# Kernel tuning notes

Measured on AMD Instinct MI355X. Metric: run time of the kernel, lower is better.

The kernel has to match this reference:

```python
import jax, jax.numpy as jnp
import numpy as np

DIM = 192
NUM_HEADS = 6
WH, WW = 7, 7
N = WH * WW  # 49 tokens per window
C2 = 2 * DIM  # concatenated channel dim = 384
SCALE = (DIM // NUM_HEADS) ** -0.5  # module uses dim//num_heads, not C2//num_heads
NW = 64  # number of windows per image
B_ = 2048  # num_windows * batch


def _relative_position_index():
    ch = np.arange(WH)
    cw = np.arange(WW)
    coords = np.stack(np.meshgrid(ch, cw, indexing='ij')).reshape(2, -1)  # [2, N]
    rel = coords[:, :, None] - coords[:, None, :]  # [2, N, N]
    rel = rel.transpose(1, 2, 0).astype(np.int64)  # [N, N, 2]
    rel[..., 0] += WH - 1
    rel[..., 1] += WW - 1
    rel[..., 0] *= 2 * WW - 1
    return jnp.asarray(rel.sum(-1))  # [N, N]

REL_IDX = _relative_position_index()


def setup_inputs() -> dict:
    key = jax.random.key(0)
    ks = jax.random.split(key, 8)
    x = jax.random.normal(ks[0], (B_, N, DIM), dtype=jnp.float32)
    y = jax.random.normal(ks[1], (B_, N, DIM), dtype=jnp.float32)
    mask = jax.random.normal(ks[2], (NW, N, N), dtype=jnp.float32)
    w_qkv = jax.random.normal(ks[3], (6 * DIM, C2), dtype=jnp.float32) * 0.02
    b_qkv = jnp.zeros((6 * DIM,), dtype=jnp.float32)
    w_proj = jax.random.normal(ks[4], (DIM, C2), dtype=jnp.float32) * 0.02
    b_proj = jnp.zeros((DIM,), dtype=jnp.float32)
    bias_table = jax.random.normal(ks[5], ((2 * WH - 1) * (2 * WW - 1), NUM_HEADS), dtype=jnp.float32) * 0.02
    return {"x": x, "y": y, "mask": mask, "w_qkv": w_qkv, "b_qkv": b_qkv,
            "w_proj": w_proj, "b_proj": b_proj, "bias_table": bias_table}


def reference(x, y, mask, w_qkv, b_qkv, w_proj, b_proj, bias_table):
    Bc = x.shape[0]
    Dh = C2 // NUM_HEADS  # 64
    xy = jnp.concatenate([x, y], axis=2)  # [B_, N, 2*dim]
    qkv = xy @ w_qkv.T + b_qkv  # [B_, N, 6*dim]
    qkv = qkv.reshape(Bc, N, 3, NUM_HEADS, Dh).transpose(2, 0, 3, 1, 4)  # [3, B_, H, N, Dh]
    q, k, v = qkv[0] * SCALE, qkv[1], qkv[2]
    attn = jnp.einsum('bhnd,bhmd->bhnm', q, k)  # [B_, H, N, N]
    rpb = bias_table[REL_IDX]  # [N, N, H]
    attn = attn + rpb.transpose(2, 0, 1)[None]
    nW = mask.shape[0]
    attn = attn.reshape(Bc // nW, nW, NUM_HEADS, N, N) + mask[None, :, None]
    attn = attn.reshape(Bc, NUM_HEADS, N, N)
    attn = jax.nn.softmax(attn, axis=-1)
    out = jnp.einsum('bhnm,bhmd->bhnd', attn, v)  # [B_, H, N, Dh]
    out = out.transpose(0, 2, 1, 3).reshape(Bc, N, C2)
    return out @ w_proj.T + b_proj  # [B_, N, dim]
```

## Files before the change

### kernel.cpp

```cpp
#include <hip/hip_runtime.h>
#include <hip/hip_bf16.h>


typedef __attribute__((ext_vector_type(8))) short short8;
typedef __attribute__((ext_vector_type(4))) float f32x4;

#define SCALE 0.17677669529663687f

#define WQF_OFF    0ul
#define WQF_BYTES  (864ul*1024)
#define WPF_OFF    (WQF_OFF + WQF_BYTES)
#define WPF_BYTES  (144ul*1024)
#define COMB_OFF   (WPF_OFF + WPF_BYTES)
#define COMB_BYTES (64ul*6*4096*4)
#define XYF_OFF    (COMB_OFF + COMB_BYTES)
#define XYF_BYTES  (2048ul*48*1024)
#define OF_OFF     (XYF_OFF + XYF_BYTES)
#define OF_BYTES   XYF_BYTES
#define WS_NEED    (OF_OFF + OF_BYTES)

__device__ __forceinline__ unsigned short f2bf(float f){
  unsigned u = __builtin_bit_cast(unsigned, f);
  u = u + 0x7fffu + ((u >> 16) & 1u);
  return (unsigned short)(u >> 16);
}
__device__ __forceinline__ unsigned long long pack4(float4 v){
  return (unsigned long long)f2bf(v.x) | ((unsigned long long)f2bf(v.y) << 16)
       | ((unsigned long long)f2bf(v.z) << 32) | ((unsigned long long)f2bf(v.w) << 48);
}

__global__ void k0_wfrag(const float* __restrict__ wq_f, const float* __restrict__ wp_f,
                         unsigned short* __restrict__ wqf, unsigned short* __restrict__ wpf){
  int t = blockIdx.x*256 + threadIdx.x;
  int fragidx = t >> 6, l = t & 63;
  const float* src; unsigned short* dst;
  if (fragidx < 864){
    int h = fragidx/144, rem = fragidx - h*144;
    int ct = rem/12, kt = rem - ct*12;
    int row = (ct>>2)*384 + h*64 + (ct&3)*16 + (l&15);
    src = wq_f + (long)row*384 + kt*32 + (l>>4)*8;
    dst = wqf + (long)fragidx*512 + l*8;
  } else {
    int fid = fragidx - 864;
    int ct = fid/12, kt = fid - ct*12;
    int row = ct*16 + (l&15);
    src = wp_f + (long)row*384 + kt*32 + (l>>4)*8;
    dst = wpf + (long)fid*512 + l*8;
  }
  short8 v;
  #pragma unroll
  for (int e = 0; e < 8; ++e) v[e] = (short)f2bf(src[e]);
  *(short8*)dst = v;
}

__global__ void prep_comb(const float* __restrict__ mask, const float* __restrict__ btab,
                          float* __restrict__ comb){
  int idx = blockIdx.x * 256 + threadIdx.x;
  int j = idx & 63, i = (idx >> 6) & 63, rest = idx >> 12;
  int h = rest % 6, w = rest / 6;
  float v;
  if (i < 49 && j < 49){
    int di = i / 7 - j / 7 + 6;
    int dj = i % 7 - j % 7 + 6;
    v = btab[(di * 13 + dj) * 6 + h] + mask[(w * 49 + i) * 49 + j];
  } else {
    v = (j >= 49) ? -1e30f : 0.0f;
  }
  comb[idx] = v;
}

__global__ void k1_xyfrag(const float* __restrict__ x, const float* __restrict__ y,
                          unsigned short* __restrict__ xyf){
  const int kt  = blockIdx.x;
  const int win = blockIdx.y;
  const int mt  = threadIdx.x >> 6;
  const int l   = threadIdx.x & 63;
  const int row = mt*16 + (l & 15);
  const int c0  = kt*32 + (l >> 4)*8;
  short8 v = {};
  if (row < 49){
    const float* src = (kt < 6) ? (x + ((long)win*49 + row)*192 + c0)
                                : (y + ((long)win*49 + row)*192 + (c0 - 192));
    float4 f0 = *(const float4*)src, f1 = *(const float4*)(src+4);
    unsigned long long lo = pack4(f0), hi = pack4(f1);
    #pragma unroll
    for (int e = 0; e < 4; ++e){ v[e] = (short)(lo >> (16*e)); v[4+e] = (short)(hi >> (16*e)); }
  }
  *(short8*)(xyf + (((long)win*12 + kt)*4 + mt)*512 + l*8) = v;
}

__device__ __forceinline__ int swz(int r, int b){ return b ^ ((r & 7) << 4); }
__device__ __forceinline__ int a_q (int r, int c){ return 0     + swz(r, r*128 + c*2); }
__device__ __forceinline__ int a_k (int r, int c){ return 8192  + swz(r, r*128 + c*2); }
__device__ __forceinline__ int a_vt(int r, int c){ return 16384 + swz(r, r*128 + c*2); }
__device__ __forceinline__ int a_p (int r, int c){ return 24576 + swz(r, r*128 + c*2); }

__global__ __launch_bounds__(256, 3)
void k2_qkv_attn(const unsigned short* __restrict__ xyf, const unsigned short* __restrict__ wqf,
                 const float* __restrict__ bqkv, const float* __restrict__ comb,
                 unsigned short* __restrict__ Of){
  __shared__ __align__(16) unsigned char smem[32768];
  const int h = blockIdx.x, win = blockIdx.y;
  const int tid = threadIdx.x, w = tid>>6, l = tid&63, l15 = l&15, lg = l>>4;

  const float* cb = comb + ((long)((win & 63)*6 + h))*4096;
  float cbv[16];
  #pragma unroll
  for (int j = 0; j < 4; ++j)
    #pragma unroll
    for (int nt = 0; nt < 4; ++nt)
      cbv[j*4+nt] = cb[(w*16 + lg*4 + j)*64 + nt*16 + l15];
  float bias[3];
  #pragma unroll
  for (int nt = 0; nt < 3; ++nt){
    int n = w*48 + nt*16 + l15;
    bias[nt] = bqkv[(n>>6)*384 + h*64 + (n&63)];
  }

  f32x4 acc[4][3] = {};
  const unsigned short* Ab = xyf + (long)win*24576;
  const unsigned short* Bb = wqf + ((long)h*12 + w*3)*12*512;
  #pragma unroll 3
  for (int kt = 0; kt < 12; ++kt){
    short8 a[4];
    #pragma unroll
    for (int mt = 0; mt < 4; ++mt)
      a[mt] = *(const short8*)(Ab + (kt*4 + mt)*512 + l*8);
    #pragma unroll
    for (int nt = 0; nt < 3; ++nt){
      short8 bb = *(const short8*)(Bb + (nt*12 + kt)*512 + l*8);
      #pragma unroll
      for (int mt = 0; mt < 4; ++mt)
        acc[mt][nt] = __builtin_amdgcn_mfma_f32_16x16x32_bf16(a[mt], bb, acc[mt][nt], 0, 0, 0);
    }
  }
  #pragma unroll
  for (int nt = 0; nt < 3; ++nt){
    int ct = w*3 + nt, s = ct>>2, d = (ct&3)*16 + l15;
    #pragma unroll
    for (int mt = 0; mt < 4; ++mt){
      #pragma unroll
      for (int j = 0; j < 4; ++j){
        int row = mt*16 + lg*4 + j;
        float v = acc[mt][nt][j] + bias[nt];
        if (s == 0) v *= SCALE;
        int addr = (s==0) ? a_q(row,d) : (s==1) ? a_k(row,d) : a_vt(d,row);
        *(unsigned short*)(smem + addr) = f2bf(v);
      }
    }
  }
  __syncthreads();

  short8 aq[2];
  #pragma unroll
  for (int ks = 0; ks < 2; ++ks)
    aq[ks] = *(const short8*)(smem + a_q(w*16 + l15, ks*32 + lg*8));
  f32x4 sacc[4] = {};
  #pragma unroll
  for (int ks = 0; ks < 2; ++ks){
    #pragma unroll
    for (int nt = 0; nt < 4; ++nt){
      short8 bk = *(const short8*)(smem + a_k(nt*16 + l15, ks*32 + lg*8));
      sacc[nt] = __builtin_amdgcn_mfma_f32_16x16x32_bf16(aq[ks], bk, sacc[nt], 0, 0, 0);
    }
  }
  float rs[4];
  #pragma unroll
  for (int j = 0; j < 4; ++j){
    int r = w*16 + lg*4 + j;
    #pragma unroll
    for (int nt = 0; nt < 4; ++nt)
      sacc[nt][j] += cbv[j*4+nt];
    float m = fmaxf(fmaxf(sacc[0][j], sacc[1][j]), fmaxf(sacc[2][j], sacc[3][j]));
    #pragma unroll
    for (int dlt = 1; dlt < 16; dlt <<= 1) m = fmaxf(m, __shfl_xor(m, dlt));
    float ssum = 0.f;
    #pragma unroll
    for (int nt = 0; nt < 4; ++nt){
      float e = __expf(sacc[nt][j] - m);
      sacc[nt][j] = e;
      ssum += e;
    }
    #pragma unroll
    for (int dlt = 1; dlt < 16; dlt <<= 1) ssum += __shfl_xor(ssum, dlt);
    rs[j] = ssum;
    #pragma unroll
    for (int nt = 0; nt < 4; ++nt)
      *(unsigned short*)(smem + a_p(r, nt*16 + l15)) = f2bf(sacc[nt][j]);
  }
  short8 ap[2];
  #pragma unroll
  for (int ks = 0; ks < 2; ++ks)
    ap[ks] = *(const short8*)(smem + a_p(w*16 + l15, ks*32 + lg*8));
  f32x4 oacc[4] = {};
  #pragma unroll
  for (int ks = 0; ks < 2; ++ks){
    #pragma unroll
    for (int nt = 0; nt < 4; ++nt){
      short8 bv = *(const short8*)(smem + a_vt(nt*16 + l15, ks*32 + lg*8));
      oacc[nt] = __builtin_amdgcn_mfma_f32_16x16x32_bf16(ap[ks], bv, oacc[nt], 0, 0, 0);
    }
  }
  float inv[4];
  #pragma unroll
  for (int j = 0; j < 4; ++j) inv[j] = 1.0f / rs[j];
  #pragma unroll
  for (int nt = 0; nt < 4; ++nt){
    #pragma unroll
    for (int j = 0; j < 4; ++j){
      int row = w*16 + lg*4 + j;
      *(unsigned short*)(smem + a_p(row, nt*16 + l15)) = f2bf(oacc[nt][j] * inv[j]);
    }
  }
  unsigned short* Ob = Of + (((long)win*12 + h*2)*4 + w)*512 + l*8;
  #pragma unroll
  for (int ks = 0; ks < 2; ++ks){
    short8 o8 = *(const short8*)(smem + a_p(w*16 + l15, ks*32 + lg*8));
    *(short8*)(Ob + ks*4*512) = o8;
  }
}

__global__ __launch_bounds__(256, 4)
void k3_proj(const unsigned short* __restrict__ Of, const unsigned short* __restrict__ wpf,
             const float* __restrict__ bproj, float* __restrict__ out){
  const int win = blockIdx.x;
  const int tid = threadIdx.x, w = tid>>6, l = tid&63, l15 = l&15, lg = l>>4;
  float bp[3]; int np[3];
  #pragma unroll
  for (int nt = 0; nt < 3; ++nt){
    np[nt] = w*48 + nt*16 + l15;
    bp[nt] = bproj[np[nt]];
  }
  f32x4 acc[4][3] = {};
  const unsigned short* Ab = Of + (long)win*24576;
  const unsigned short* Bb = wpf + (long)(w*3)*12*512;
  #pragma unroll 3
  for (int kt = 0; kt < 12; ++kt){
    short8 a[4];
    #pragma unroll
    for (int mt = 0; mt < 4; ++mt)
      a[mt] = *(const short8*)(Ab + (kt*4 + mt)*512 + l*8);
    #pragma unroll
    for (int nt = 0; nt < 3; ++nt){
      short8 bb = *(const short8*)(Bb + (nt*12 + kt)*512 + l*8);
      #pragma unroll
      for (int mt = 0; mt < 4; ++mt)
        acc[mt][nt] = __builtin_amdgcn_mfma_f32_16x16x32_bf16(a[mt], bb, acc[mt][nt], 0, 0, 0);
    }
  }
  #pragma unroll
  for (int mt = 0; mt < 4; ++mt){
    #pragma unroll
    for (int j = 0; j < 4; ++j){
      int row = mt*16 + lg*4 + j;
      if (row < 49){
        float* o = out + ((long)win*49 + row)*192;
        #pragma unroll
        for (int nt = 0; nt < 3; ++nt)
          o[np[nt]] = acc[mt][nt][j] + bp[nt];
      }
    }
  }
}

#define FB_WQ_ELEMS (1152*384)
#define FB_WP_ELEMS (192*384)
#define FB_WP_OFF   (FB_WQ_ELEMS*2)
#define FB_COMB_OFF (FB_WP_OFF + FB_WP_ELEMS*2)

__global__ void prep_weights_fb(const float* __restrict__ wq_f, const float* __restrict__ wp_f,
                                unsigned short* __restrict__ wq, unsigned short* __restrict__ wp){
  int gid = blockIdx.x * 256 + threadIdx.x;
  if (gid < FB_WQ_ELEMS) wq[gid] = f2bf(wq_f[gid]);
  else { int g = gid - FB_WQ_ELEMS; if (g < FB_WP_ELEMS) wp[g] = f2bf(wp_f[g]); }
}
__device__ __forceinline__ int fb_xy(int r, int c){ return 0      + swz(r, r*768 + c*2); }
__device__ __forceinline__ int fb_q (int r, int c){ return 49152  + swz(r, r*128 + c*2); }
__device__ __forceinline__ int fb_k (int r, int c){ return 57344  + swz(r, r*128 + c*2); }
__device__ __forceinline__ int fb_vt(int r, int c){ return 65536  + swz(r, r*128 + c*2); }
__device__ __forceinline__ int fb_p (int r, int c){ return 73728  + swz(r, r*128 + c*2); }

__global__ __launch_bounds__(256, 2)
void fused_attn_fb(const float* __restrict__ x, const float* __restrict__ y,
                   const float* __restrict__ bqkv, const float* __restrict__ bproj,
                   const unsigned short* __restrict__ wq, const unsigned short* __restrict__ wp,
                   const float* __restrict__ comb, float* __restrict__ out){
  __shared__ __align__(16) unsigned char smem[81920];
  const int b = blockIdx.x, tid = threadIdx.x;
  const int w = tid>>6, l = tid&63, l15 = l&15, lg = l>>4;
  {
    const float4* x4 = (const float4*)x + b * 2352;
    const float4* y4 = (const float4*)y + b * 2352;
    for (int idx = tid; idx < 2352; idx += 256){
      int r = idx / 48, c4 = (idx % 48) * 4;
      float4 vx = x4[idx], vy = y4[idx];
      *(unsigned long long*)(smem + fb_xy(r, c4))       = pack4(vx);
      *(unsigned long long*)(smem + fb_xy(r, 192 + c4)) = pack4(vy);
    }
    for (int idx = tid; idx < 1440; idx += 256){
      int r = 49 + idx / 96, c4 = (idx % 96) * 4;
      *(unsigned long long*)(smem + fb_xy(r, c4)) = 0ull;
    }
  }
  __syncthreads();
  const float* cbB = comb + (long)(b & 63) * (6 * 4096);
  f32x4 pacc[4][3] = {};
  int np[3]; float bp[3];
  #pragma unroll
  for (int nt = 0; nt < 3; ++nt){ np[nt] = w*48 + nt*16 + l15; bp[nt] = bproj[np[nt]]; }
  #pragma unroll 1
  for (int h = 0; h < 6; ++h){
    f32x4 acc[4][3] = {};
    int wrow[3]; float bias[3];
    #pragma unroll
    for (int nt = 0; nt < 3; ++nt){
      int n = np[nt];
      wrow[nt] = (n >> 6) * 384 + h * 64 + (n & 63);
      bias[nt] = bqkv[wrow[nt]];
    }
    #pragma unroll 4
    for (int kt = 0; kt < 12; ++kt){
      int k0 = kt * 32;
      short8 a[4];
      #pragma unroll
      for (int mt = 0; mt < 4; ++mt)
        a[mt] = *(const short8*)(smem + fb_xy(mt*16 + l15, k0 + lg*8));
      #pragma unroll
      for (int nt = 0; nt < 3; ++nt){
        short8 bb = *(const short8*)(wq + (long)wrow[nt]*384 + k0 + lg*8);
        #pragma unroll
        for (int mt = 0; mt < 4; ++mt)
          acc[mt][nt] = __builtin_amdgcn_mfma_f32_16x16x32_bf16(a[mt], bb, acc[mt][nt], 0, 0, 0);
      }
    }
    #pragma unroll
    for (int nt = 0; nt < 3; ++nt){
      int n = np[nt], s = n >> 6, d = n & 63;
      #pragma unroll
      for (int mt = 0; mt < 4; ++mt){
        #pragma unroll
        for (int j = 0; j < 4; ++j){
          int row = mt*16 + lg*4 + j;
          float v = acc[mt][nt][j] + bias[nt];
          if (s == 0) v *= SCALE;
          int addr = (s==0) ? fb_q(row,d) : (s==1) ? fb_k(row,d) : fb_vt(d,row);
          *(unsigned short*)(smem + addr) = f2bf(v);
        }
      }
    }
    __syncthreads();
    short8 aq[2];
    #pragma unroll
    for (int ks = 0; ks < 2; ++ks)
      aq[ks] = *(const short8*)(smem + fb_q(w*16 + l15, ks*32 + lg*8));
    f32x4 sacc[4] = {};
    #pragma unroll
    for (int ks = 0; ks < 2; ++ks)
      #pragma unroll
      for (int nt = 0; nt < 4; ++nt){
        short8 bk = *(const short8*)(smem + fb_k(nt*16 + l15, ks*32 + lg*8));
        sacc[nt] = __builtin_amdgcn_mfma_f32_16x16x32_bf16(aq[ks], bk, sacc[nt], 0, 0, 0);
      }
    const float* cb = cbB + h * 4096;
    float rs[4];
    #pragma unroll
    for (int j = 0; j < 4; ++j){
      int r = w*16 + lg*4 + j;
      #pragma unroll
      for (int nt = 0; nt < 4; ++nt) sacc[nt][j] += cb[r*64 + nt*16 + l15];
      float m = fmaxf(fmaxf(sacc[0][j], sacc[1][j]), fmaxf(sacc[2][j], sacc[3][j]));
      #pragma unroll
      for (int dlt = 1; dlt < 16; dlt <<= 1) m = fmaxf(m, __shfl_xor(m, dlt));
      float ssum = 0.f;
      #pragma unroll
      for (int nt = 0; nt < 4; ++nt){
        float e = __expf(sacc[nt][j] - m);
        sacc[nt][j] = e; ssum += e;
      }
      #pragma unroll
      for (int dlt = 1; dlt < 16; dlt <<= 1) ssum += __shfl_xor(ssum, dlt);
      rs[j] = ssum;
      #pragma unroll
      for (int nt = 0; nt < 4; ++nt)
        *(unsigned short*)(smem + fb_p(r, nt*16 + l15)) = f2bf(sacc[nt][j]);
    }
    short8 ap[2];
    #pragma unroll
    for (int ks = 0; ks < 2; ++ks)
      ap[ks] = *(const short8*)(smem + fb_p(w*16 + l15, ks*32 + lg*8));
    f32x4 oacc[4] = {};
    #pragma unroll
    for (int ks = 0; ks < 2; ++ks)
      #pragma unroll
      for (int nt = 0; nt < 4; ++nt){
        short8 bv = *(const short8*)(smem + fb_vt(nt*16 + l15, ks*32 + lg*8));
        oacc[nt] = __builtin_amdgcn_mfma_f32_16x16x32_bf16(ap[ks], bv, oacc[nt], 0, 0, 0);
      }
    float inv[4];
    #pragma unroll
    for (int j = 0; j < 4; ++j) inv[j] = 1.0f / rs[j];
    #pragma unroll
    for (int nt = 0; nt < 4; ++nt)
      #pragma unroll
      for (int j = 0; j < 4; ++j){
        int row = w*16 + lg*4 + j;
        *(unsigned short*)(smem + fb_p(row, nt*16 + l15)) = f2bf(oacc[nt][j] * inv[j]);
      }
    __syncthreads();
    #pragma unroll
    for (int ks = 0; ks < 2; ++ks){
      short8 ao8[4];
      #pragma unroll
      for (int mt = 0; mt < 4; ++mt)
        ao8[mt] = *(const short8*)(smem + fb_p(mt*16 + l15, ks*32 + lg*8));
      #pragma unroll
      for (int nt = 0; nt < 3; ++nt){
        short8 bb = *(const short8*)(wp + (long)np[nt]*384 + h*64 + ks*32 + lg*8);
        #pragma unroll
        for (int mt = 0; mt < 4; ++mt)
          pacc[mt][nt] = __builtin_amdgcn_mfma_f32_16x16x32_bf16(ao8[mt], bb, pacc[mt][nt], 0, 0, 0);
      }
    }
  }
  #pragma unroll
  for (int mt = 0; mt < 4; ++mt)
    #pragma unroll
    for (int j = 0; j < 4; ++j){
      int row = mt*16 + lg*4 + j;
      if (row < 49){
        float* o = out + ((long)b*49 + row)*192;
        #pragma unroll
        for (int nt = 0; nt < 3; ++nt)
          o[np[nt]] = pacc[mt][nt][j] + bp[nt];
      }
    }
}

extern "C" void kernel_launch(void* const* d_in, const int* in_sizes, int n_in,
                              void* d_out, int out_size, void* d_ws, size_t ws_size,
                              hipStream_t stream){
  (void)in_sizes; (void)n_in; (void)out_size;
  const float* x     = (const float*)d_in[0];
  const float* y     = (const float*)d_in[1];
  const float* mask  = (const float*)d_in[2];
  const float* wq_f  = (const float*)d_in[3];
  const float* bqkv  = (const float*)d_in[4];
  const float* wp_f  = (const float*)d_in[5];
  const float* bproj = (const float*)d_in[6];
  const float* btab  = (const float*)d_in[7];
  float* out = (float*)d_out;

  if (ws_size >= WS_NEED){
    unsigned short* wqf = (unsigned short*)((char*)d_ws + WQF_OFF);
    unsigned short* wpf = (unsigned short*)((char*)d_ws + WPF_OFF);
    float*          cmb = (float*)((char*)d_ws + COMB_OFF);
    unsigned short* xyf = (unsigned short*)((char*)d_ws + XYF_OFF);
    unsigned short* Ofr = (unsigned short*)((char*)d_ws + OF_OFF);
    hipLaunchKernelGGL(k0_wfrag,    dim3(252),     dim3(256), 0, stream, wq_f, wp_f, wqf, wpf);
    hipLaunchKernelGGL(prep_comb,   dim3(6144),    dim3(256), 0, stream, mask, btab, cmb);
    hipLaunchKernelGGL(k1_xyfrag,   dim3(12,2048), dim3(256), 0, stream, x, y, xyf);
    hipLaunchKernelGGL(k2_qkv_attn, dim3(6,2048),  dim3(256), 0, stream, xyf, wqf, bqkv, cmb, Ofr);
    hipLaunchKernelGGL(k3_proj,     dim3(2048),    dim3(256), 0, stream, Ofr, wpf, bproj, out);
  } else {
    unsigned short* wq  = (unsigned short*)d_ws;
    unsigned short* wp  = (unsigned short*)((char*)d_ws + FB_WP_OFF);
    float*          cmb = (float*)((char*)d_ws + FB_COMB_OFF);
    hipLaunchKernelGGL(prep_weights_fb, dim3(2016), dim3(256), 0, stream, wq_f, wp_f, wq, wp);
    hipLaunchKernelGGL(prep_comb,       dim3(6144), dim3(256), 0, stream, mask, btab, cmb);
    hipLaunchKernelGGL(fused_attn_fb,   dim3(2048), dim3(256), 0, stream,
                       x, y, bqkv, bproj, wq, wp, cmb, out);
  }
}
```

Before: 275.4 us.

## Transpose score MFMA, reuse Q smem for P, raise occupancy, remap blocks across XCDs

The attention kernel now computes S^T via swapped MFMA operands, so each lane holds a full column of scores. This lets the softmax reduce with two cross-lane shuffles instead of four-step reductions and write P and V^T with packed 8-byte stores. P and the output now reuse the Q region of shared memory, shrinking LDS to 24KB and raising launch bounds to 6 blocks/SM; the mask+bias load moves after the QKV GEMM as float4 loads to cut register pressure. Grids are flattened and block IDs remapped so consecutive windows spread across the 8 XCDs, trading some L2 locality assumptions for balance.

```diff
diff --git a/kernel.cpp b/kernel.cpp
--- a/kernel.cpp
+++ b/kernel.cpp
@@ -71,8 +71,9 @@
 
 __global__ void k1_xyfrag(const float* __restrict__ x, const float* __restrict__ y,
                           unsigned short* __restrict__ xyf){
-  const int kt  = blockIdx.x;
-  const int win = blockIdx.y;
+  const int id = blockIdx.x;
+  const int p  = (id & 7) * 3072 + (id >> 3);
+  const int win = p / 12, kt = p - win * 12;
   const int mt  = threadIdx.x >> 6;
   const int l   = threadIdx.x & 63;
   const int row = mt*16 + (l & 15);
@@ -93,23 +94,18 @@
 __device__ __forceinline__ int a_q (int r, int c){ return 0     + swz(r, r*128 + c*2); }
 __device__ __forceinline__ int a_k (int r, int c){ return 8192  + swz(r, r*128 + c*2); }
 __device__ __forceinline__ int a_vt(int r, int c){ return 16384 + swz(r, r*128 + c*2); }
-__device__ __forceinline__ int a_p (int r, int c){ return 24576 + swz(r, r*128 + c*2); }
-
-__global__ __launch_bounds__(256, 3)
+
+__global__ __launch_bounds__(256, 6)
 void k2_qkv_attn(const unsigned short* __restrict__ xyf, const unsigned short* __restrict__ wqf,
                  const float* __restrict__ bqkv, const float* __restrict__ comb,
                  unsigned short* __restrict__ Of){
-  __shared__ __align__(16) unsigned char smem[32768];
-  const int h = blockIdx.x, win = blockIdx.y;
+  __shared__ __align__(16) unsigned char smem[24576];
+  const int id  = blockIdx.x;
+  const int pr  = (id & 7) * 1536 + (id >> 3);
+  const int win = pr / 6;
+  const int h   = pr - win * 6;
   const int tid = threadIdx.x, w = tid>>6, l = tid&63, l15 = l&15, lg = l>>4;
 
-  const float* cb = comb + ((long)((win & 63)*6 + h))*4096;
-  float cbv[16];
-  #pragma unroll
-  for (int j = 0; j < 4; ++j)
-    #pragma unroll
-    for (int nt = 0; nt < 4; ++nt)
-      cbv[j*4+nt] = cb[(w*16 + lg*4 + j)*64 + nt*16 + l15];
   float bias[3];
   #pragma unroll
   for (int nt = 0; nt < 3; ++nt){
@@ -134,64 +130,91 @@
         acc[mt][nt] = __builtin_amdgcn_mfma_f32_16x16x32_bf16(a[mt], bb, acc[mt][nt], 0, 0, 0);
     }
   }
+
+  const float* cb = comb + ((long)((win & 63)*6 + h))*4096 + (w*16 + l15)*64 + lg*4;
+  float4 cbv[4];
+  #pragma unroll
+  for (int nt = 0; nt < 4; ++nt) cbv[nt] = *(const float4*)(cb + nt*16);
+
   #pragma unroll
   for (int nt = 0; nt < 3; ++nt){
-    int ct = w*3 + nt, s = ct>>2, d = (ct&3)*16 + l15;
-    #pragma unroll
-    for (int mt = 0; mt < 4; ++mt){
-      #pragma unroll
-      for (int j = 0; j < 4; ++j){
-        int row = mt*16 + lg*4 + j;
-        float v = acc[mt][nt][j] + bias[nt];
-        if (s == 0) v *= SCALE;
-        int addr = (s==0) ? a_q(row,d) : (s==1) ? a_k(row,d) : a_vt(d,row);
-        *(unsigned short*)(smem + addr) = f2bf(v);
+    int ct = w*3 + nt, s = ct >> 2, d16 = (ct & 3) * 16;
+    if (s == 2){
+      #pragma unroll
+      for (int mt = 0; mt < 4; ++mt){
+        float4 vv;
+        vv.x = acc[mt][nt][0] + bias[nt]; vv.y = acc[mt][nt][1] + bias[nt];
+        vv.z = acc[mt][nt][2] + bias[nt]; vv.w = acc[mt][nt][3] + bias[nt];
+        *(unsigned long long*)(smem + a_vt(d16 + l15, mt*16 + lg*4)) = pack4(vv);
+      }
+    } else {
+      float sc = (s == 0) ? SCALE : 1.0f;
+      #pragma unroll
+      for (int mt = 0; mt < 4; ++mt){
+        #pragma unroll
+        for (int j = 0; j < 4; ++j){
+          int row = mt*16 + lg*4 + j;
+          float v = (acc[mt][nt][j] + bias[nt]) * sc;
+          int addr = (s == 0) ? a_q(row, d16 + l15) : a_k(row, d16 + l15);
+          *(unsigned short*)(smem + addr) = f2bf(v);
+        }
       }
     }
   }
   __syncthreads();
 
-  short8 aq[2];
+  short8 bq[2];
   #pragma unroll
   for (int ks = 0; ks < 2; ++ks)
-    aq[ks] = *(const short8*)(smem + a_q(w*16 + l15, ks*32 + lg*8));
-  f32x4 sacc[4] = {};
+    bq[ks] = *(const short8*)(smem + a_q(w*16 + l15, ks*32 + lg*8));
+  f32x4 st[4] = {};
   #pragma unroll
   for (int ks = 0; ks < 2; ++ks){
     #pragma unroll
     for (int nt = 0; nt < 4; ++nt){
-      short8 bk = *(const short8*)(smem + a_k(nt*16 + l15, ks*32 + lg*8));
-      sacc[nt] = __builtin_amdgcn_mfma_f32_16x16x32_bf16(aq[ks], bk, sacc[nt], 0, 0, 0);
-    }
-  }
-  float rs[4];
-  #pragma unroll
-  for (int j = 0; j < 4; ++j){
-    int r = w*16 + lg*4 + j;
-    #pragma unroll
-    for (int nt = 0; nt < 4; ++nt)
-      sacc[nt][j] += cbv[j*4+nt];
-    float m = fmaxf(fmaxf(sacc[0][j], sacc[1][j]), fmaxf(sacc[2][j], sacc[3][j]));
-    #pragma unroll
-    for (int dlt = 1; dlt < 16; dlt <<= 1) m = fmaxf(m, __shfl_xor(m, dlt));
-    float ssum = 0.f;
-    #pragma unroll
-    for (int nt = 0; nt < 4; ++nt){
-      float e = __expf(sacc[nt][j] - m);
-      sacc[nt][j] = e;
-      ssum += e;
-    }
-    #pragma unroll
-    for (int dlt = 1; dlt < 16; dlt <<= 1) ssum += __shfl_xor(ssum, dlt);
-    rs[j] = ssum;
-    #pragma unroll
-    for (int nt = 0; nt < 4; ++nt)
-      *(unsigned short*)(smem + a_p(r, nt*16 + l15)) = f2bf(sacc[nt][j]);
-  }
+      short8 ak = *(const short8*)(smem + a_k(nt*16 + l15, ks*32 + lg*8));
+      st[nt] = __builtin_amdgcn_mfma_f32_16x16x32_bf16(ak, bq[ks], st[nt], 0, 0, 0);
+    }
+  }
+  #pragma unroll
+  for (int nt = 0; nt < 4; ++nt){
+    st[nt][0] += cbv[nt].x; st[nt][1] += cbv[nt].y;
+    st[nt][2] += cbv[nt].z; st[nt][3] += cbv[nt].w;
+  }
+  float mx;
+  {
+    float m0 = fmaxf(fmaxf(st[0][0], st[0][1]), fmaxf(st[0][2], st[0][3]));
+    float m1 = fmaxf(fmaxf(st[1][0], st[1][1]), fmaxf(st[1][2], st[1][3]));
+    float m2 = fmaxf(fmaxf(st[2][0], st[2][1]), fmaxf(st[2][2], st[2][3]));
+    float m3 = fmaxf(fmaxf(st[3][0], st[3][1]), fmaxf(st[3][2], st[3][3]));
+    mx = fmaxf(fmaxf(m0, m1), fmaxf(m2, m3));
+  }
+  mx = fmaxf(mx, __shfl_xor(mx, 16));
+  mx = fmaxf(mx, __shfl_xor(mx, 32));
+  float ssum = 0.f;
+  #pragma unroll
+  for (int nt = 0; nt < 4; ++nt){
+    #pragma unroll
+    for (int j = 0; j < 4; ++j){
+      float e = __expf(st[nt][j] - mx);
+      st[nt][j] = e; ssum += e;
+    }
+  }
+  ssum += __shfl_xor(ssum, 16);
+  ssum += __shfl_xor(ssum, 32);
+  const float inv = 1.0f / ssum;
+
+  #pragma unroll
+  for (int nt = 0; nt < 4; ++nt){
+    float4 vv;
+    vv.x = st[nt][0]*inv; vv.y = st[nt][1]*inv; vv.z = st[nt][2]*inv; vv.w = st[nt][3]*inv;
+    *(unsigned long long*)(smem + a_q(w*16 + l15, nt*16 + lg*4)) = pack4(vv);
+  }
+
   short8 ap[2];
   #pragma unroll
   for (int ks = 0; ks < 2; ++ks)
-    ap[ks] = *(const short8*)(smem + a_p(w*16 + l15, ks*32 + lg*8));
+    ap[ks] = *(const short8*)(smem + a_q(w*16 + l15, ks*32 + lg*8));
   f32x4 oacc[4] = {};
   #pragma unroll
   for (int ks = 0; ks < 2; ++ks){
@@ -201,21 +224,16 @@
       oacc[nt] = __builtin_amdgcn_mfma_f32_16x16x32_bf16(ap[ks], bv, oacc[nt], 0, 0, 0);
     }
   }
-  float inv[4];
-  #pragma unroll
-  for (int j = 0; j < 4; ++j) inv[j] = 1.0f / rs[j];
   #pragma unroll
   for (int nt = 0; nt < 4; ++nt){
     #pragma unroll
-    for (int j = 0; j < 4; ++j){
-      int row = w*16 + lg*4 + j;
-      *(unsigned short*)(smem + a_p(row, nt*16 + l15)) = f2bf(oacc[nt][j] * inv[j]);
-    }
+    for (int j = 0; j < 4; ++j)
+      *(unsigned short*)(smem + a_q(w*16 + lg*4 + j, nt*16 + l15)) = f2bf(oacc[nt][j]);
   }
   unsigned short* Ob = Of + (((long)win*12 + h*2)*4 + w)*512 + l*8;
   #pragma unroll
   for (int ks = 0; ks < 2; ++ks){
-    short8 o8 = *(const short8*)(smem + a_p(w*16 + l15, ks*32 + lg*8));
+    short8 o8 = *(const short8*)(smem + a_q(w*16 + l15, ks*32 + lg*8));
     *(short8*)(Ob + ks*4*512) = o8;
   }
 }
@@ -223,7 +241,8 @@
 __global__ __launch_bounds__(256, 4)
 void k3_proj(const unsigned short* __restrict__ Of, const unsigned short* __restrict__ wpf,
              const float* __restrict__ bproj, float* __restrict__ out){
-  const int win = blockIdx.x;
+  const int id  = blockIdx.x;
+  const int win = (id & 7) * 256 + (id >> 3);
   const int tid = threadIdx.x, w = tid>>6, l = tid&63, l15 = l&15, lg = l>>4;
   float bp[3]; int np[3];
   #pragma unroll
@@ -456,11 +475,11 @@
     float*          cmb = (float*)((char*)d_ws + COMB_OFF);
     unsigned short* xyf = (unsigned short*)((char*)d_ws + XYF_OFF);
     unsigned short* Ofr = (unsigned short*)((char*)d_ws + OF_OFF);
-    hipLaunchKernelGGL(k0_wfrag,    dim3(252),     dim3(256), 0, stream, wq_f, wp_f, wqf, wpf);
-    hipLaunchKernelGGL(prep_comb,   dim3(6144),    dim3(256), 0, stream, mask, btab, cmb);
-    hipLaunchKernelGGL(k1_xyfrag,   dim3(12,2048), dim3(256), 0, stream, x, y, xyf);
-    hipLaunchKernelGGL(k2_qkv_attn, dim3(6,2048),  dim3(256), 0, stream, xyf, wqf, bqkv, cmb, Ofr);
-    hipLaunchKernelGGL(k3_proj,     dim3(2048),    dim3(256), 0, stream, Ofr, wpf, bproj, out);
+    hipLaunchKernelGGL(k0_wfrag,    dim3(252),   dim3(256), 0, stream, wq_f, wp_f, wqf, wpf);
+    hipLaunchKernelGGL(prep_comb,   dim3(6144),  dim3(256), 0, stream, mask, btab, cmb);
+    hipLaunchKernelGGL(k1_xyfrag,   dim3(24576), dim3(256), 0, stream, x, y, xyf);
+    hipLaunchKernelGGL(k2_qkv_attn, dim3(12288), dim3(256), 0, stream, xyf, wqf, bqkv, cmb, Ofr);
+    hipLaunchKernelGGL(k3_proj,     dim3(2048),  dim3(256), 0, stream, Ofr, wpf, bproj, out);
   } else {
     unsigned short* wq  = (unsigned short*)d_ws;
     unsigned short* wp  = (unsigned short*)((char*)d_ws + FB_WP_OFF);
```

After: 476.5 us. +73.0%, slower.
